# Performance work log

Measured on AMD Instinct MI355X. Metric: run time of the kernel, lower is better.

Reference implementation:

```python
import jax, jax.numpy as jnp
import numpy as np

D_MODEL = 256
NUM_HEADS = 8
HEAD_DIM = D_MODEL // NUM_HEADS
B, L = 2, 2048


def setup_inputs() -> dict:
    key = jax.random.key(0)
    ks = jax.random.split(key, 16)
    s = 0.02
    return {
        "query": jax.random.normal(ks[0], (B, L, D_MODEL), jnp.float32),
        "key": jax.random.normal(ks[1], (B, L, D_MODEL), jnp.float32),
        "value": jax.random.normal(ks[2], (B, L, D_MODEL), jnp.float32),
        "struct_bias": jax.random.normal(ks[3], (B, NUM_HEADS, L, L), jnp.float32),
        "attn_mask": jax.random.normal(ks[4], (B, NUM_HEADS, L, L), jnp.float32),
        "Wq": jax.random.normal(ks[5], (D_MODEL, D_MODEL), jnp.float32) * s,
        "bq": jnp.zeros((D_MODEL,), jnp.float32),
        "Wk": jax.random.normal(ks[6], (D_MODEL, D_MODEL), jnp.float32) * s,
        "bk": jnp.zeros((D_MODEL,), jnp.float32),
        "Wv": jax.random.normal(ks[7], (D_MODEL, D_MODEL), jnp.float32) * s,
        "bv": jnp.zeros((D_MODEL,), jnp.float32),
        "Wo": jax.random.normal(ks[8], (D_MODEL, D_MODEL), jnp.float32) * s,
        "bo": jnp.zeros((D_MODEL,), jnp.float32),
    }


def reference(query, key, value, struct_bias, attn_mask,
              Wq, bq, Wk, bk, Wv, bv, Wo, bo):
    b, t, _ = query.shape
    # projections (torch Linear: x @ W.T + b)
    q = query @ Wq.T + bq
    k = key @ Wk.T + bk
    v = value @ Wv.T + bv
    # [B, H, L, Dh]
    q = q.reshape(b, t, NUM_HEADS, HEAD_DIM).transpose(0, 2, 1, 3)
    k = k.reshape(b, t, NUM_HEADS, HEAD_DIM).transpose(0, 2, 1, 3)
    v = v.reshape(b, t, NUM_HEADS, HEAD_DIM).transpose(0, 2, 1, 3)
    scale = 1.0 / np.sqrt(HEAD_DIM).astype(np.float32)
    scores = jnp.einsum("bhqd,bhkd->bhqk", q, k) * scale
    scores = scores + struct_bias + attn_mask
    attn_weights = jax.nn.softmax(scores, axis=-1)
    context = jnp.einsum("bhqk,bhkd->bhqd", attn_weights, v)
    context = context.transpose(0, 2, 1, 3).reshape(b, t, D_MODEL)
    output = context @ Wo.T + bo
    return (output, attn_weights)
```

## Files before the change

### kernel.cpp

```cpp
#include <hip/hip_runtime.h>

typedef __bf16 bf16x8 __attribute__((ext_vector_type(8)));
typedef short  s16x8  __attribute__((ext_vector_type(8)));
typedef float  f32x4  __attribute__((ext_vector_type(4)));

#define MFMA16(a,b,c) __builtin_amdgcn_mfma_f32_16x16x32_bf16((a),(b),(c),0,0,0)

static constexpr float SCALE = 0.17677669529663687f;

__device__ __forceinline__ unsigned short f2b(float f){
  __bf16 h = (__bf16)f;
  return __builtin_bit_cast(unsigned short, h);
}
__device__ __forceinline__ bf16x8 ldfrag(const unsigned short* p){
  s16x8 v = *(const s16x8*)p;
  return __builtin_bit_cast(bf16x8, v);
}
__device__ __forceinline__ bf16x8 cvt8(const float* p){
  f32x4 a = *(const f32x4*)p;
  f32x4 b = *(const f32x4*)(p+4);
  bf16x8 r;
  r[0]=(__bf16)a[0]; r[1]=(__bf16)a[1]; r[2]=(__bf16)a[2]; r[3]=(__bf16)a[3];
  r[4]=(__bf16)b[0]; r[5]=(__bf16)b[1]; r[6]=(__bf16)b[2]; r[7]=(__bf16)b[3];
  return r;
}

__global__ __launch_bounds__(256) void proj_kernel(
    const float* __restrict__ xq, const float* __restrict__ xk, const float* __restrict__ xv,
    const float* __restrict__ Wq, const float* __restrict__ bq,
    const float* __restrict__ Wk, const float* __restrict__ bk,
    const float* __restrict__ Wv, const float* __restrict__ bv,
    unsigned short* __restrict__ qo, unsigned short* __restrict__ ko,
    unsigned short* __restrict__ vT)
{
  const int z = blockIdx.z;
  const float* x    = (z==0) ? xq : (z==1 ? xk : xv);
  const float* W    = (z==0) ? Wq : (z==1 ? Wk : Wv);
  const float* bias = (z==0) ? bq : (z==1 ? bk : bv);
  const int tid = threadIdx.x, w = tid>>6, l = tid&63;
  const int m0 = blockIdx.x*16;
  const int n0 = blockIdx.y*64 + w*16;
  const int ra = l&15, ko8 = (l>>4)*8;

  __shared__ unsigned short xs[16*264];
  #pragma unroll
  for(int i=0;i<4;++i){
    int chunk = tid + i*256;
    int row = chunk>>6, c4 = (chunk&63)*4;
    f32x4 v = *(const f32x4*)(x + (m0+row)*256 + c4);
    ushort4 u; u.x=f2b(v[0]); u.y=f2b(v[1]); u.z=f2b(v[2]); u.w=f2b(v[3]);
    *(ushort4*)(&xs[row*264 + c4]) = u;
  }
  __syncthreads();

  f32x4 acc = {0.f,0.f,0.f,0.f};
  #pragma unroll
  for(int kk=0;kk<8;++kk){
    int kb = kk*32 + ko8;
    bf16x8 a   = ldfrag(&xs[ra*264 + kb]);
    bf16x8 bfr = cvt8(W + (n0+ra)*256 + kb);
    acc = MFMA16(a, bfr, acc);
  }
  const int col = l&15;
  const int n = n0 + col;
  const float bval = bias[n];

  __shared__ float vt[4][16][17];
  if(z < 2){
    unsigned short* out = (z==0) ? qo : ko;
    #pragma unroll
    for(int r=0;r<4;++r){
      int R = (l>>4)*4 + r, m = m0 + R;
      float val = acc[r] + bval;
      if(z==0) val *= SCALE;
      int bidx = m>>11, ls = m&2047, hh = n>>5, dh = n&31;
      out[(((long)(bidx*8+hh))*2048 + ls)*32 + dh] = f2b(val);
    }
  } else {
    #pragma unroll
    for(int r=0;r<4;++r){
      int R = (l>>4)*4 + r;
      vt[w][R][col] = acc[r] + bval;
    }
    __syncthreads();
    int bidx = m0>>11, hh = n0>>5, dh0 = n0&31, bh = bidx*8 + hh;
    int lsc = m0 & 2047;
    int dloc = l>>2, kloc = (l&3)*4;
    ushort4 pk;
    pk.x = f2b(vt[w][kloc+0][dloc]);
    pk.y = f2b(vt[w][kloc+1][dloc]);
    pk.z = f2b(vt[w][kloc+2][dloc]);
    pk.w = f2b(vt[w][kloc+3][dloc]);
    *reinterpret_cast<ushort4*>(vT + ((long)(bh*32 + dh0 + dloc))*2048 + lsc + kloc) = pk;
  }
}

__global__ __launch_bounds__(1024) void attn_kernel(
    const unsigned short* __restrict__ qbf, const unsigned short* __restrict__ kbf,
    const unsigned short* __restrict__ vT,
    const float* __restrict__ sbias, const float* __restrict__ amask,
    float* __restrict__ Pout, float* __restrict__ ctx)
{
  __shared__ float sS[16*2048];
  __shared__ float linv[16];

  const int tid = threadIdx.x, w = tid>>6, l = tid&63;
  const int q0 = blockIdx.x*16;
  const int h = blockIdx.y, b = blockIdx.z;
  const int bh = b*8 + h;
  const long qkbase = (long)bh*2048*32;
  const long vbase  = (long)bh*32*2048;
  const long bmbase = ((long)bh*2048 + q0)*2048;
  const long rowbase = bmbase + (long)w*2048;
  const int ws = w*128;
  const int col = l&15, ko8 = (l>>4)*8, rg = (l>>4)*4;
  const int swzw = (w&7)<<2;
  const f32x4 zero = {0.f,0.f,0.f,0.f};

  bf16x8 aq = ldfrag(qbf + qkbase + (long)(q0+col)*32 + ko8);
  bf16x8 kf[8];
  #pragma unroll
  for(int t=0;t<8;++t)
    kf[t] = ldfrag(kbf + qkbase + (long)(ws + t*16 + col)*32 + ko8);

  f32x4 s[8];
  #pragma unroll
  for(int k=0;k<8;++k){
    long c = rowbase + k*256 + l*4;
    f32x4 b4 = __builtin_nontemporal_load((const f32x4*)(sbias + c));
    f32x4 m4 = __builtin_nontemporal_load((const f32x4*)(amask + c));
    s[k] = b4 + m4;
  }

  #pragma unroll
  for(int t=0;t<8;++t){
    int key0 = ws + t*16;
    f32x4 acc = MFMA16(aq, kf[t], zero);
    #pragma unroll
    for(int r=0;r<4;++r){
      int R = rg + r;
      sS[R*2048 + ((key0+col) ^ ((R&7)<<2))] = acc[r];
    }
  }

  bf16x8 vf0[4], vf1[4];
  #pragma unroll
  for(int c4=0;c4<4;++c4){
    int kb = ws + c4*32 + ko8;
    vf0[c4] = ldfrag(vT + vbase + (long)col*2048 + kb);
    vf1[c4] = ldfrag(vT + vbase + (long)(16+col)*2048 + kb);
  }
  __syncthreads();

  float m = -1e30f;
  #pragma unroll
  for(int k=0;k<8;++k){
    int c = k*256 + l*4;
    f32x4 v = *(const f32x4*)(&sS[w*2048 + (c ^ swzw)]);
    s[k][0]+=v[0]; s[k][1]+=v[1]; s[k][2]+=v[2]; s[k][3]+=v[3];
    m = fmaxf(m, fmaxf(fmaxf(s[k][0],s[k][1]), fmaxf(s[k][2],s[k][3])));
  }
  #pragma unroll
  for(int d=1;d<64;d<<=1) m = fmaxf(m, __shfl_xor(m, d));
  float sum = 0.f;
  #pragma unroll
  for(int k=0;k<8;++k){
    s[k][0]=__expf(s[k][0]-m); s[k][1]=__expf(s[k][1]-m);
    s[k][2]=__expf(s[k][2]-m); s[k][3]=__expf(s[k][3]-m);
    sum += (s[k][0]+s[k][1]) + (s[k][2]+s[k][3]);
  }
  #pragma unroll
  for(int d=1;d<64;d<<=1) sum += __shfl_xor(sum, d);
  const float li = 1.0f/sum;
  if(l==0) linv[w] = li;

  #pragma unroll
  for(int k=0;k<8;++k){
    int c = k*256 + l*4;
    f32x4 p; p[0]=s[k][0]*li; p[1]=s[k][1]*li; p[2]=s[k][2]*li; p[3]=s[k][3]*li;
    __builtin_nontemporal_store(p, (f32x4*)(Pout + rowbase + c));
    *(f32x4*)(&sS[w*2048 + (c ^ swzw)]) = s[k];
  }
  __syncthreads();

  f32x4 acc0 = zero, acc1 = zero;
  #pragma unroll
  for(int c4=0;c4<4;++c4){
    int kb = ws + c4*32 + ko8;
    f32x4 e0 = *(const f32x4*)(&sS[col*2048 + ( kb    ^ ((col&7)<<2))]);
    f32x4 e1 = *(const f32x4*)(&sS[col*2048 + ((kb+4) ^ ((col&7)<<2))]);
    bf16x8 pa;
    pa[0]=(__bf16)e0[0]; pa[1]=(__bf16)e0[1]; pa[2]=(__bf16)e0[2]; pa[3]=(__bf16)e0[3];
    pa[4]=(__bf16)e1[0]; pa[5]=(__bf16)e1[1]; pa[6]=(__bf16)e1[2]; pa[7]=(__bf16)e1[3];
    acc0 = MFMA16(pa, vf0[c4], acc0);
    acc1 = MFMA16(pa, vf1[c4], acc1);
  }
  __syncthreads();

  #pragma unroll
  for(int r=0;r<4;++r){
    int R = rg + r;
    sS[w*512 + R*32 + col]      = acc0[r];
    sS[w*512 + R*32 + 16 + col] = acc1[r];
  }
  __syncthreads();
  if(tid < 512){
    int row = tid>>5, dh = tid&31;
    float ssum = 0.f;
    #pragma unroll
    for(int w2=0; w2<16; ++w2) ssum += sS[w2*512 + row*32 + dh];
    ctx[((long)b*2048 + q0 + row)*256 + h*32 + dh] = ssum * linv[row];
  }
}

__global__ __launch_bounds__(256) void oproj_kernel(
    float* __restrict__ out0, const float* __restrict__ Wo, const float* __restrict__ bo)
{
  __shared__ unsigned short lct[8*264];
  const int tid = threadIdx.x, w = tid>>6, l = tid&63;
  const int m0 = blockIdx.x*8;
  #pragma unroll
  for(int i=0;i<2;++i){
    int chunk = tid + i*256;
    int row = chunk>>6, c4 = (chunk&63)*4;
    f32x4 v = *(const f32x4*)(out0 + (m0+row)*256 + c4);
    ushort4 u; u.x=f2b(v[0]); u.y=f2b(v[1]); u.z=f2b(v[2]); u.w=f2b(v[3]);
    *(ushort4*)(&lct[row*264 + c4]) = u;
  }
  __syncthreads();
  const int col = l&15, ko8 = (l>>4)*8, rg = (l>>4)*4;
  const int arow = col&7;
  #pragma unroll
  for(int nt=0;nt<4;++nt){
    int n0 = w*64 + nt*16;
    f32x4 acc = {0.f,0.f,0.f,0.f};
    #pragma unroll
    for(int kk=0;kk<8;++kk){
      int kb = kk*32 + ko8;
      bf16x8 a   = ldfrag(&lct[arow*264 + kb]);
      bf16x8 bfr = cvt8(Wo + (n0+col)*256 + kb);
      acc = MFMA16(a, bfr, acc);
    }
    float bv = bo[n0+col];
    if(rg < 8){
      #pragma unroll
      for(int r=0;r<4;++r){
        out0[(m0+rg+r)*256 + n0+col] = acc[r] + bv;
      }
    }
  }
}

extern "C" void kernel_launch(void* const* d_in, const int* in_sizes, int n_in,
                              void* d_out, int out_size, void* d_ws, size_t ws_size,
                              hipStream_t stream)
{
  const float* query = (const float*)d_in[0];
  const float* key   = (const float*)d_in[1];
  const float* value = (const float*)d_in[2];
  const float* sbias = (const float*)d_in[3];
  const float* amask = (const float*)d_in[4];
  const float* Wq = (const float*)d_in[5];
  const float* bq = (const float*)d_in[6];
  const float* Wk = (const float*)d_in[7];
  const float* bk = (const float*)d_in[8];
  const float* Wv = (const float*)d_in[9];
  const float* bv = (const float*)d_in[10];
  const float* Wo = (const float*)d_in[11];
  const float* bo = (const float*)d_in[12];

  float* out0 = (float*)d_out;
  float* Pout = out0 + (size_t)2*2048*256;

  unsigned short* qbf = (unsigned short*)d_ws;
  unsigned short* kbf = qbf + (size_t)2*8*2048*32;
  unsigned short* vTb = kbf + (size_t)2*8*2048*32;

  proj_kernel<<<dim3(256,4,3), 256, 0, stream>>>(query,key,value,Wq,bq,Wk,bk,Wv,bv,qbf,kbf,vTb);
  attn_kernel<<<dim3(128,8,2), 1024, 0, stream>>>(qbf,kbf,vTb,sbias,amask,Pout,out0);
  oproj_kernel<<<dim3(512), 256, 0, stream>>>(out0,Wo,bo);
}
```

Before: 217.0 us.

## Store attention scores in LDS as bf16 and defer K/V fragment loads

The shared score buffer in the attention kernel changes from fp32 to bf16, halving its LDS footprint from 128KB to 64KB so more blocks can be resident per CU. K and V fragments are now loaded just before use instead of being preloaded into registers, which lowers register pressure, and launch_bounds gains a min-blocks hint. The risk is extra precision loss: raw QK scores are rounded to bf16 before bias and softmax. The V loads are also no longer overlapped with the softmax phase.

```diff
diff --git a/kernel.cpp b/kernel.cpp
--- a/kernel.cpp
+++ b/kernel.cpp
@@ -1,6 +1,7 @@
 #include <hip/hip_runtime.h>
 
 typedef __bf16 bf16x8 __attribute__((ext_vector_type(8)));
+typedef __bf16 bf16x4 __attribute__((ext_vector_type(4)));
 typedef short  s16x8  __attribute__((ext_vector_type(8)));
 typedef float  f32x4  __attribute__((ext_vector_type(4)));
 
@@ -95,13 +96,13 @@
   }
 }
 
-__global__ __launch_bounds__(1024) void attn_kernel(
+__global__ __launch_bounds__(1024, 8) void attn_kernel(
     const unsigned short* __restrict__ qbf, const unsigned short* __restrict__ kbf,
     const unsigned short* __restrict__ vT,
     const float* __restrict__ sbias, const float* __restrict__ amask,
     float* __restrict__ Pout, float* __restrict__ ctx)
 {
-  __shared__ float sS[16*2048];
+  __shared__ unsigned short sS[16*2048];
   __shared__ float linv[16];
 
   const int tid = threadIdx.x, w = tid>>6, l = tid&63;
@@ -117,12 +118,6 @@
   const int swzw = (w&7)<<2;
   const f32x4 zero = {0.f,0.f,0.f,0.f};
 
-  bf16x8 aq = ldfrag(qbf + qkbase + (long)(q0+col)*32 + ko8);
-  bf16x8 kf[8];
-  #pragma unroll
-  for(int t=0;t<8;++t)
-    kf[t] = ldfrag(kbf + qkbase + (long)(ws + t*16 + col)*32 + ko8);
-
   f32x4 s[8];
   #pragma unroll
   for(int k=0;k<8;++k){
@@ -132,23 +127,17 @@
     s[k] = b4 + m4;
   }
 
+  bf16x8 aq = ldfrag(qbf + qkbase + (long)(q0+col)*32 + ko8);
   #pragma unroll
   for(int t=0;t<8;++t){
     int key0 = ws + t*16;
-    f32x4 acc = MFMA16(aq, kf[t], zero);
+    bf16x8 bk = ldfrag(kbf + qkbase + (long)(key0+col)*32 + ko8);
+    f32x4 acc = MFMA16(aq, bk, zero);
     #pragma unroll
     for(int r=0;r<4;++r){
       int R = rg + r;
-      sS[R*2048 + ((key0+col) ^ ((R&7)<<2))] = acc[r];
-    }
-  }
-
-  bf16x8 vf0[4], vf1[4];
-  #pragma unroll
-  for(int c4=0;c4<4;++c4){
-    int kb = ws + c4*32 + ko8;
-    vf0[c4] = ldfrag(vT + vbase + (long)col*2048 + kb);
-    vf1[c4] = ldfrag(vT + vbase + (long)(16+col)*2048 + kb);
+      sS[R*2048 + ((key0+col) ^ ((R&7)<<2))] = f2b(acc[r]);
+    }
   }
   __syncthreads();
 
@@ -156,8 +145,8 @@
   #pragma unroll
   for(int k=0;k<8;++k){
     int c = k*256 + l*4;
-    f32x4 v = *(const f32x4*)(&sS[w*2048 + (c ^ swzw)]);
-    s[k][0]+=v[0]; s[k][1]+=v[1]; s[k][2]+=v[2]; s[k][3]+=v[3];
+    bf16x4 v = *(const bf16x4*)(&sS[w*2048 + (c ^ swzw)]);
+    s[k][0]+=(float)v[0]; s[k][1]+=(float)v[1]; s[k][2]+=(float)v[2]; s[k][3]+=(float)v[3];
     m = fmaxf(m, fmaxf(fmaxf(s[k][0],s[k][1]), fmaxf(s[k][2],s[k][3])));
   }
   #pragma unroll
@@ -179,36 +168,42 @@
     int c = k*256 + l*4;
     f32x4 p; p[0]=s[k][0]*li; p[1]=s[k][1]*li; p[2]=s[k][2]*li; p[3]=s[k][3]*li;
     __builtin_nontemporal_store(p, (f32x4*)(Pout + rowbase + c));
-    *(f32x4*)(&sS[w*2048 + (c ^ swzw)]) = s[k];
+    bf16x4 e4; e4[0]=(__bf16)s[k][0]; e4[1]=(__bf16)s[k][1];
+    e4[2]=(__bf16)s[k][2]; e4[3]=(__bf16)s[k][3];
+    *(bf16x4*)(&sS[w*2048 + (c ^ swzw)]) = e4;
   }
   __syncthreads();
 
   f32x4 acc0 = zero, acc1 = zero;
+  const int sw = (col&7)<<2;
   #pragma unroll
   for(int c4=0;c4<4;++c4){
     int kb = ws + c4*32 + ko8;
-    f32x4 e0 = *(const f32x4*)(&sS[col*2048 + ( kb    ^ ((col&7)<<2))]);
-    f32x4 e1 = *(const f32x4*)(&sS[col*2048 + ((kb+4) ^ ((col&7)<<2))]);
+    bf16x4 p0 = *(const bf16x4*)(&sS[col*2048 + ( kb    ^ sw)]);
+    bf16x4 p1 = *(const bf16x4*)(&sS[col*2048 + ((kb+4) ^ sw)]);
     bf16x8 pa;
-    pa[0]=(__bf16)e0[0]; pa[1]=(__bf16)e0[1]; pa[2]=(__bf16)e0[2]; pa[3]=(__bf16)e0[3];
-    pa[4]=(__bf16)e1[0]; pa[5]=(__bf16)e1[1]; pa[6]=(__bf16)e1[2]; pa[7]=(__bf16)e1[3];
-    acc0 = MFMA16(pa, vf0[c4], acc0);
-    acc1 = MFMA16(pa, vf1[c4], acc1);
-  }
-  __syncthreads();
-
+    pa[0]=p0[0]; pa[1]=p0[1]; pa[2]=p0[2]; pa[3]=p0[3];
+    pa[4]=p1[0]; pa[5]=p1[1]; pa[6]=p1[2]; pa[7]=p1[3];
+    bf16x8 v0 = ldfrag(vT + vbase + (long)col*2048 + kb);
+    bf16x8 v1 = ldfrag(vT + vbase + (long)(16+col)*2048 + kb);
+    acc0 = MFMA16(pa, v0, acc0);
+    acc1 = MFMA16(pa, v1, acc1);
+  }
+  __syncthreads();
+
+  float* sF = (float*)sS;
   #pragma unroll
   for(int r=0;r<4;++r){
     int R = rg + r;
-    sS[w*512 + R*32 + col]      = acc0[r];
-    sS[w*512 + R*32 + 16 + col] = acc1[r];
+    sF[w*512 + R*32 + col]      = acc0[r];
+    sF[w*512 + R*32 + 16 + col] = acc1[r];
   }
   __syncthreads();
   if(tid < 512){
     int row = tid>>5, dh = tid&31;
     float ssum = 0.f;
     #pragma unroll
-    for(int w2=0; w2<16; ++w2) ssum += sS[w2*512 + row*32 + dh];
+    for(int w2=0; w2<16; ++w2) ssum += sF[w2*512 + row*32 + dh];
     ctx[((long)b*2048 + q0 + row)*256 + h*32 + dh] = ssum * linv[row];
   }
 }
```

Result: slower. 235.5 us (+8.5%).
